# Kernel tuning notes

Hardware: AMD Instinct MI355X
Metric: run time of the kernel (lower is better)

## Reference

```python
import jax, jax.numpy as jnp
import numpy as np

EPS = 1e-5

def conv2d(x, w, stride=1, padding=1, dilation=1):
    # x: [N, C, H, W], w: [O, I, kh, kw]
    return jax.lax.conv_general_dilated(
        x, w, (stride, stride), [(padding, padding), (padding, padding)],
        rhs_dilation=(dilation, dilation),
        dimension_numbers=('NCHW', 'OIHW', 'NCHW'))


def setup_inputs() -> dict:
    key = jax.random.key(0)
    ks = jax.random.split(key, 7)
    T, N, Cin, H, W = 16, 4, 64, 64, 64
    Cout = 64
    x = jax.random.normal(ks[0], (T, N, Cin, H, W), dtype=jnp.float32)
    gamma = jnp.ones((Cin,), jnp.float32)
    beta = jnp.zeros((Cin,), jnp.float32)
    conv1_w = jax.random.normal(ks[1], (3 * Cout, Cin, 3, 3), jnp.float32) * 0.02
    conv1_b = jax.random.normal(ks[2], (3 * Cout,), jnp.float32) * 0.02
    w_h2h = jax.random.normal(ks[3], (3 * Cout, Cout, 3, 3), jnp.float32) * 0.02
    w_c2h = jax.random.normal(ks[4], (3 * Cout, Cout, 3, 3), jnp.float32) * 0.02
    return {"x": x, "gamma": gamma, "beta": beta, "conv1_w": conv1_w,
            "conv1_b": conv1_b, "w_h2h": w_h2h, "w_c2h": w_c2h}


def reference(x, gamma, beta, conv1_w, conv1_b, w_h2h, w_c2h):
    T, N, Cin, H, W = x.shape
    Cout = w_h2h.shape[1]
    # time_to_batch: [T, N, C, H, W] -> [T*N, C, H, W]
    xb = x.reshape(T * N, Cin, H, W)
    # BatchNorm2d (training mode: biased batch stats over N*T, H, W)
    mean = jnp.mean(xb, axis=(0, 2, 3), keepdims=True)
    var = jnp.var(xb, axis=(0, 2, 3), keepdims=True)
    g = gamma.reshape(1, Cin, 1, 1)
    b = beta.reshape(1, Cin, 1, 1)
    bnx = (xb - mean) * jax.lax.rsqrt(var + EPS) * g + b
    # conv1: Cin -> 3*Cout
    y = conv2d(bnx, conv1_w, stride=1, padding=1) + conv1_b.reshape(1, -1, 1, 1)
    # batch_to_time: -> [T, N, 3*Cout, H, W]
    y = y.reshape(T, N, 3 * Cout, H, W)

    # ConvLSTMCell: zero init state is exact (h2h/c2h convs have no bias)
    h0 = jnp.zeros((N, Cout, H, W), y.dtype)
    c0 = jnp.zeros((N, Cout, H, W), y.dtype)

    def step(carry, yt):
        h, c = carry
        tmp = conv2d(c, w_c2h, padding=1) + conv2d(h, w_h2h, padding=1) + yt
        cc_f, cc_o, cc_g = jnp.split(tmp, 3, axis=1)
        f = jax.nn.sigmoid(cc_f)
        o = jax.nn.sigmoid(cc_o)
        gg = jnp.tanh(cc_g)
        c_new = f * c + (1.0 - f) * gg
        h_new = o * jnp.tanh(c_new)
        return (h_new, c_new), h_new

    _, hs = jax.lax.scan(step, (h0, c0), y)
    return hs  # [T, N, Cout, H, W]
```

## Files before the change

kernel.cpp:

```cpp
#include <hip/hip_runtime.h>

typedef unsigned short u16;
typedef unsigned int   u32;
typedef __attribute__((ext_vector_type(8))) short short8;
typedef __attribute__((ext_vector_type(4))) float f32x4;

typedef __attribute__((address_space(1))) const void GASV;
typedef __attribute__((address_space(3))) void LASV;

#define IMG_BYTES  557568
#define WS_SCALE   0
#define WS_SHIFT   256
#define WS_BTAB    512
#define WS_PART2   7424
#define WS_WA      8704
#define WS_BNXP    672256
#define WS_HC      (WS_BNXP + (size_t)64*IMG_BYTES)
#define WS_CSTATE  (WS_HC + (size_t)16*IMG_BYTES)
#define WS_PARTB   (WS_CSTATE + 4194304ULL)

#define SM_RING_OFF 33792
#define SMEM_TOT    (33792 + 6*12288)

__device__ __forceinline__ u16 f2b(float f){
  u32 x = __float_as_uint(f);
  return (u16)((x + 0x7fffu + ((x>>16)&1u)) >> 16);
}
__device__ __forceinline__ float b2f(u16 u){ return __uint_as_float(((u32)u)<<16); }
__device__ __forceinline__ float sigm(float x){ return 1.f/(1.f+__expf(-x)); }
__device__ __forceinline__ float tanh_(float x){
  float e = __expf(2.f*fabsf(x));
  float t = 1.f - 2.f/(e+1.f);
  return copysignf(t, x);
}

__global__ void k_wt(const float* __restrict__ c1, const float* __restrict__ c2h,
                     const float* __restrict__ h2h, const float* __restrict__ scale,
                     u16* __restrict__ wA){
  int idx = blockIdx.x*256 + threadIdx.x;
  int e = idx & 7;
  int lane = (idx >> 3) & 63;
  int v = idx >> 9;
  int f2 = v % 12;  v /= 12;
  int oh = v & 1;
  int stage = v >> 1;
  int cc = f2 / 6, gate = (f2 % 6) >> 1, og2 = f2 & 1;
  int j = stage / 9, tap = stage % 9;
  int och = gate*64 + (oh*2 + og2)*16 + (lane & 15);
  int c = cc*32 + (lane >> 4)*8 + e;
  const float* src = (j==0) ? c1 : ((j==1) ? c2h : h2h);
  float vv = src[(och*64 + c)*9 + tap];
  if (j == 0) vv *= scale[c];
  wA[idx] = f2b(vv);
}

__global__ void k_xt(const float* __restrict__ x, char* __restrict__ xp){
  int img = blockIdx.x / 66, rp = blockIdx.x % 66;
  int tid = threadIdx.x;
  char* dstrow = xp + (size_t)img*IMG_BYTES + (size_t)rp*8448;
  const uint4 z = {0,0,0,0};
  if (rp == 0 || rp == 65){
    for (int i = tid; i < 528; i += 256) ((uint4*)dstrow)[i] = z;
    return;
  }
  if (tid < 16)
    *(uint4*)(dstrow + (tid>>3)*(65*128) + (tid&7)*16) = z;
  int r = rp - 1;
  int col = tid & 63, cq = tid >> 6;
  const float* xb = x + (((size_t)(img*64 + cq*16)) << 12) + (r<<6) + col;
  union { u16 u[16]; uint4 v[2]; } pk;
  #pragma unroll
  for (int i = 0; i < 16; ++i)
    pk.u[i] = f2b(xb[((size_t)i) << 12]);
  char* dst = dstrow + (size_t)(col + 1)*128 + cq*32;
  *(uint4*)dst = pk.v[0];
  *(uint4*)(dst+16) = pk.v[1];
}

__global__ void k_stats(const char* __restrict__ xp, float* __restrict__ part){
  int img = blockIdx.x >> 2, rq = blockIdx.x & 3;
  int tid = threadIdx.x;
  int ch = tid & 7, cell0 = tid >> 3;
  float s[8], q[8];
  #pragma unroll
  for (int i = 0; i < 8; ++i){ s[i] = 0.f; q[i] = 0.f; }
  const char* base = xp + (size_t)img*IMG_BYTES + (size_t)(rq*16+1)*8448 + 128;
  for (int p = 0; p < 32; ++p){
    int cell = p*32 + cell0;
    int rr = cell >> 6, cc = cell & 63;
    uint4 v = *(const uint4*)(base + (size_t)rr*8448 + (size_t)cc*128 + ch*16);
    const u16* u = (const u16*)&v;
    #pragma unroll
    for (int i = 0; i < 8; ++i){
      float f = b2f(u[i]);
      s[i] += f; q[i] += f*f;
    }
  }
  #pragma unroll
  for (int i = 0; i < 8; ++i){
    #pragma unroll
    for (int off = 8; off < 64; off <<= 1){
      s[i] += __shfl_down(s[i], off);
      q[i] += __shfl_down(q[i], off);
    }
  }
  __shared__ float red[4][8][17];
  int w = tid >> 6, lane = tid & 63;
  if (lane < 8){
    #pragma unroll
    for (int i = 0; i < 8; ++i){
      red[w][lane][i]   = s[i];
      red[w][lane][8+i] = q[i];
    }
  }
  __syncthreads();
  if (tid < 128){
    int c = tid & 63, sq = tid >> 6;
    float acc = 0.f;
    #pragma unroll
    for (int wv = 0; wv < 4; ++wv)
      acc += red[wv][c>>3][sq*8 + (c&7)];
    part[(size_t)blockIdx.x*128 + sq*64 + c] = acc;
  }
}

__global__ void k_red(const float* __restrict__ part, float* __restrict__ part2){
  int b = blockIdx.x;
  float s = part[(size_t)threadIdx.x*128 + b];
  #pragma unroll
  for (int off = 32; off; off >>= 1) s += __shfl_down(s, off);
  __shared__ float red[4];
  int w = threadIdx.x >> 6, lane = threadIdx.x & 63;
  if (lane == 0) red[w] = s;
  __syncthreads();
  if (threadIdx.x == 0) part2[b] = red[0]+red[1]+red[2]+red[3];
}

__global__ void k_bnfin(const float* __restrict__ part2, const float* __restrict__ gamma,
                        const float* __restrict__ beta, float* __restrict__ scale,
                        float* __restrict__ shift){
  int c = threadIdx.x;
  const float inv = 1.f/262144.f;
  float mean = part2[c]*inv;
  float var  = part2[64+c]*inv - mean*mean;
  float sc = gamma[c] * rsqrtf(var + 1e-5f);
  scale[c] = sc;
  shift[c] = beta[c] - mean*sc;
}

__global__ void k_bias(const float* __restrict__ c1w, const float* __restrict__ c1b,
                       const float* __restrict__ shift, float* __restrict__ btab){
  int o = blockIdx.x, c = threadIdx.x;
  const float* wp = c1w + (o*64 + c)*9;
  float sh = shift[c];
  float tap[9];
  #pragma unroll
  for (int k = 0; k < 9; ++k) tap[k] = sh*wp[k];
  #pragma unroll
  for (int k = 0; k < 9; ++k){
    #pragma unroll
    for (int off = 32; off; off >>= 1)
      tap[k] += __shfl_down(tap[k], off);
  }
  if (c == 0){
    float b = c1b[o];
    #pragma unroll
    for (int cls = 0; cls < 9; ++cls){
      int rc = cls/3, cl = cls%3;
      int kh0 = (rc==0)?1:0, kh1 = (rc==2)?1:2;
      int kw0 = (cl==0)?1:0, kw1 = (cl==2)?1:2;
      float sm = b;
      for (int kh = kh0; kh <= kh1; ++kh)
        for (int kw = kw0; kw <= kw1; ++kw)
          sm += tap[kh*3+kw];
      btab[cls*192 + o] = sm;
    }
  }
}

#define STAGE_W(v) do {                                                         \
  if ((v) <= 26 && w < 4){                                                      \
    int _vj = jp + (v)/9; if (_vj >= 3) _vj -= 3;                               \
    int _vt = tp + (v)%9; if (_vt >= 9) _vt -= 9;                               \
    const char* _gs = wA + ((size_t)((_vj*9 + _vt)*2 + oh))*12288               \
                        + w*3072 + lane*16;                                     \
    char* _ls = smem + SM_RING_OFF + ((v)%6)*12288 + w*3072;                    \
    __builtin_amdgcn_global_load_lds((GASV*)(_gs),        (LASV*)(_ls),        16, 0, 0); \
    __builtin_amdgcn_global_load_lds((GASV*)(_gs + 1024), (LASV*)(_ls + 1024), 16, 0, 0); \
    __builtin_amdgcn_global_load_lds((GASV*)(_gs + 2048), (LASV*)(_ls + 2048), 16, 0, 0); \
  }                                                                             \
} while(0)

#define WAITN_BAR(N) do {                                                       \
  asm volatile("s_waitcnt vmcnt(" #N ")\n\ts_barrier" ::: "memory");            \
  __builtin_amdgcn_sched_barrier(0);                                            \
} while(0)

#define COMPUTE(u) do {                                                         \
  int tv = tp + (u)%9; if (tv >= 9) tv -= 9;                                    \
  const int kh = tv/3, kw = tv - kh*3;                                          \
  const char* ab0 = smem + SM_RING_OFF + ((u)%6)*12288 + og2*1024 + lane*16;    \
  const int c_ = (ch<<5) + kw + l15;                                            \
  const char* rowb = smem + (wr + kh)*8448 + c_*128;                            \
  _Pragma("unroll")                                                             \
  for (int cc = 0; cc < 2; ++cc){                                               \
    short8 af = *(const short8*)(ab0 + cc*6144);                                \
    short8 ao = *(const short8*)(ab0 + cc*6144 + 2048);                         \
    short8 ag = *(const short8*)(ab0 + cc*6144 + 4096);                         \
    const char* ib0 = rowb + ((((cc<<2)|l4) ^ (c_&7))<<4);                      \
    _Pragma("unroll")                                                           \
    for (int cf = 0; cf < 2; ++cf){                                             \
      short8 bf = *(const short8*)(ib0 + (cf<<11));                             \
      acc[0][cf] = __builtin_amdgcn_mfma_f32_16x16x32_bf16(af, bf, acc[0][cf], 0,0,0); \
      acc[1][cf] = __builtin_amdgcn_mfma_f32_16x16x32_bf16(ao, bf, acc[1][cf], 0,0,0); \
      acc[2][cf] = __builtin_amdgcn_mfma_f32_16x16x32_bf16(ag, bf, acc[2][cf], 0,0,0); \
    }                                                                           \
  }                                                                             \
} while(0)

__global__ __launch_bounds__(512, 1) void k_step(
    const char* __restrict__ bnxp,
    const char* __restrict__ cpad_s, const char* __restrict__ hpad_s,
    char* __restrict__ cpad_d, char* __restrict__ hpad_d,
    const char* __restrict__ wA, const float* __restrict__ btab,
    float* __restrict__ cstate, float* __restrict__ out, int t)
{
  extern __shared__ __align__(16) char smem[];
  const int tid = threadIdx.x;
  const int w = tid >> 6, lane = tid & 63;
  const int l15 = lane & 15, l4 = lane >> 4;
  const int wr = w >> 2, og2 = (w >> 1) & 1, ch = w & 1;
  const int bid = blockIdx.x;
  const int oh = bid & 1, rp = (bid >> 1) & 31, n = bid >> 6;
  const int jp = bid % 3, tp = bid % 9;
  const int r = (rp << 1) + wr;

  const char* gb0 = bnxp   + (size_t)(t*4+n)*IMG_BYTES + rp*16896;
  const char* gb1 = cpad_s + (size_t)n*IMG_BYTES + rp*16896;
  const char* gb2 = hpad_s + (size_t)n*IMG_BYTES + rp*16896;

  float* cslot = cstate + ((size_t)bid*512 + tid)*8;
  float cpv[8];
  if (t == 0){
    #pragma unroll
    for (int i = 0; i < 8; ++i) cpv[i] = 0.f;
  } else {
    f32x4 c0 = *(const f32x4*)cslot;
    f32x4 c1v = *(const f32x4*)(cslot + 4);
    cpv[0]=c0[0]; cpv[1]=c0[1]; cpv[2]=c0[2]; cpv[3]=c0[3];
    cpv[4]=c1v[0]; cpv[5]=c1v[1]; cpv[6]=c1v[2]; cpv[7]=c1v[3];
  }

  const int gc0 = ((oh<<1) + og2)*16 + l4*4;
  const int rc = (r==0) ? 0 : ((r==63) ? 2 : 1);
  const float* btr = btab + rc*576;
  float bv2[2][12];
  #pragma unroll
  for (int cf = 0; cf < 2; ++cf){
    const int col = (ch<<5) + (cf<<4) + l15;
    const int ccl = (col==0) ? 0 : ((col==63) ? 2 : 1);
    const float* bb = btr + ccl*192;
    #pragma unroll
    for (int reg = 0; reg < 4; ++reg){
      bv2[cf][reg]   = bb[gc0+reg];
      bv2[cf][4+reg] = bb[64+gc0+reg];
      bv2[cf][8+reg] = bb[128+gc0+reg];
    }
  }

  f32x4 acc[3][2];
  #pragma unroll
  for (int a = 0; a < 3; ++a)
    #pragma unroll
    for (int b = 0; b < 2; ++b)
      acc[a][b] = (f32x4){0.f,0.f,0.f,0.f};

  STAGE_W(0); STAGE_W(1); STAGE_W(2); STAGE_W(3);

  #pragma unroll
  for (int jj = 0; jj < 3; ++jj){
    int jv = jp + jj; if (jv >= 3) jv -= 3;
    const char* gbj = (jv==0) ? gb0 : ((jv==1) ? gb1 : gb2);
    for (int i = tid; i < 2112; i += 512){
      int rr = i / 528;
      int iw = i - rr*528;
      int c = iw >> 3, k = iw & 7;
      *(uint4*)(smem + rr*8448 + c*128 + ((k ^ (c&7))<<4)) =
          *(const uint4*)(gbj + rr*8448 + iw*16);
    }
    __syncthreads();

    #pragma unroll
    for (int pp = 0; pp < 4; ++pp){
      const int u = jj*9 + 2*pp;
      STAGE_W(u+4); STAGE_W(u+5);
      __builtin_amdgcn_s_setprio(1);
      COMPUTE(u);
      COMPUTE(u+1);
      __builtin_amdgcn_s_setprio(0);
      if (u == 22)      WAITN_BAR(3);
      else if (u == 24) WAITN_BAR(0);
      else              WAITN_BAR(6);
    }
    {
      const int u = jj*9 + 8;
      STAGE_W(u+4);
      __builtin_amdgcn_s_setprio(1);
      COMPUTE(u);
      __builtin_amdgcn_s_setprio(0);
    }
  }

  const size_t ob = ((size_t)((t*4+n)*64)) << 12;
  char* hrow = hpad_d + (size_t)n*IMG_BYTES + (size_t)(r+1)*8448;
  char* crow = cpad_d + (size_t)n*IMG_BYTES + (size_t)(r+1)*8448;

  float cnew[8];
  #pragma unroll
  for (int cf = 0; cf < 2; ++cf){
    const int col = (ch<<5) + (cf<<4) + l15;
    const int p = (r<<6) + col;
    union { u16 u[4]; uint2 v; } hp, cp2;
    #pragma unroll
    for (int reg = 0; reg < 4; ++reg){
      const int gc = gc0 + reg;
      float f  = sigm(acc[0][cf][reg] + bv2[cf][reg]);
      float og_ = sigm(acc[1][cf][reg] + bv2[cf][4+reg]);
      float g  = tanh_(acc[2][cf][reg] + bv2[cf][8+reg]);
      float cn = f*cpv[cf*4+reg] + (1.f-f)*g;
      float hn = og_ * tanh_(cn);
      cnew[cf*4+reg] = cn;
      out[ob + (((size_t)gc)<<12) + p] = hn;
      hp.u[reg]  = f2b(hn);
      cp2.u[reg] = f2b(cn);
    }
    *(uint2*)(hrow + (size_t)(col+1)*128 + gc0*2) = hp.v;
    *(uint2*)(crow + (size_t)(col+1)*128 + gc0*2) = cp2.v;
  }
  *(f32x4*)cslot       = (f32x4){cnew[0],cnew[1],cnew[2],cnew[3]};
  *(f32x4*)(cslot + 4) = (f32x4){cnew[4],cnew[5],cnew[6],cnew[7]};
}

extern "C" void kernel_launch(void* const* d_in, const int* in_sizes, int n_in,
                              void* d_out, int out_size, void* d_ws, size_t ws_size,
                              hipStream_t stream)
{
  (void)in_sizes; (void)n_in; (void)out_size; (void)ws_size;
  const float* x     = (const float*)d_in[0];
  const float* gamma = (const float*)d_in[1];
  const float* beta  = (const float*)d_in[2];
  const float* c1w   = (const float*)d_in[3];
  const float* c1b   = (const float*)d_in[4];
  const float* wh2h  = (const float*)d_in[5];
  const float* wc2h  = (const float*)d_in[6];
  char* ws  = (char*)d_ws;
  float* out = (float*)d_out;

  hipFuncSetAttribute(reinterpret_cast<const void*>(k_step),
                      hipFuncAttributeMaxDynamicSharedMemorySize, SMEM_TOT);

  char* hpad0 = ws + WS_HC;
  char* cpad0 = ws + WS_HC + (size_t)4*IMG_BYTES;
  char* hpad1 = ws + WS_HC + (size_t)8*IMG_BYTES;
  char* cpad1 = ws + WS_HC + (size_t)12*IMG_BYTES;

  hipMemsetAsync(ws + WS_HC, 0, (size_t)16*IMG_BYTES, stream);

  k_xt<<<4224, 256, 0, stream>>>(x, ws + WS_BNXP);
  k_stats<<<256, 256, 0, stream>>>(ws + WS_BNXP, (float*)(ws + WS_PARTB));
  k_red<<<128, 256, 0, stream>>>((const float*)(ws + WS_PARTB),
                                 (float*)(ws + WS_PART2));
  k_bnfin<<<1, 64, 0, stream>>>((const float*)(ws + WS_PART2), gamma, beta,
                                (float*)(ws + WS_SCALE), (float*)(ws + WS_SHIFT));
  k_wt<<<1296, 256, 0, stream>>>(c1w, wc2h, wh2h,
                                 (const float*)(ws + WS_SCALE), (u16*)(ws + WS_WA));
  k_bias<<<192, 64, 0, stream>>>(c1w, c1b, (const float*)(ws + WS_SHIFT),
                                 (float*)(ws + WS_BTAB));

  for (int t = 0; t < 16; ++t){
    const char* cs = (t & 1) ? cpad1 : cpad0;
    const char* hs = (t & 1) ? hpad1 : hpad0;
    char* cd = (t & 1) ? cpad0 : cpad1;
    char* hd = (t & 1) ? hpad0 : hpad1;
    k_step<<<256, 512, SMEM_TOT, stream>>>(ws + WS_BNXP, cs, hs, cd, hd,
                                           ws + WS_WA,
                                           (const float*)(ws + WS_BTAB),
                                           (float*)(ws + WS_CSTATE), out, t);
  }
}
```

Before: 356.2 us.

## Drop LDS staging in step kernel; load weights and inputs straight from global

Removes the shared-memory ring that staged weights and the swizzled shared-memory copy of the input rows. Each wave now loads its A fragments (weights) into registers with double buffering and reads B fragments directly from global memory, with no barriers. This removes the LDS copy traffic and synchronisation cost. The trade-off is that every wave issues redundant global and L2 reads of the same weights and overlapping input rows, and exposes global load latency in front of the MFMAs.

```diff
diff --git a/kernel.cpp b/kernel.cpp
--- a/kernel.cpp
+++ b/kernel.cpp
@@ -4,9 +4,6 @@
 typedef unsigned int   u32;
 typedef __attribute__((ext_vector_type(8))) short short8;
 typedef __attribute__((ext_vector_type(4))) float f32x4;
-
-typedef __attribute__((address_space(1))) const void GASV;
-typedef __attribute__((address_space(3))) void LASV;
 
 #define IMG_BYTES  557568
 #define WS_SCALE   0
@@ -18,9 +15,6 @@
 #define WS_HC      (WS_BNXP + (size_t)64*IMG_BYTES)
 #define WS_CSTATE  (WS_HC + (size_t)16*IMG_BYTES)
 #define WS_PARTB   (WS_CSTATE + 4194304ULL)
-
-#define SM_RING_OFF 33792
-#define SMEM_TOT    (33792 + 6*12288)
 
 __device__ __forceinline__ u16 f2b(float f){
   u32 x = __float_as_uint(f);
@@ -178,42 +172,33 @@
   }
 }
 
-#define STAGE_W(v) do {                                                         \
-  if ((v) <= 26 && w < 4){                                                      \
-    int _vj = jp + (v)/9; if (_vj >= 3) _vj -= 3;                               \
-    int _vt = tp + (v)%9; if (_vt >= 9) _vt -= 9;                               \
-    const char* _gs = wA + ((size_t)((_vj*9 + _vt)*2 + oh))*12288               \
-                        + w*3072 + lane*16;                                     \
-    char* _ls = smem + SM_RING_OFF + ((v)%6)*12288 + w*3072;                    \
-    __builtin_amdgcn_global_load_lds((GASV*)(_gs),        (LASV*)(_ls),        16, 0, 0); \
-    __builtin_amdgcn_global_load_lds((GASV*)(_gs + 1024), (LASV*)(_ls + 1024), 16, 0, 0); \
-    __builtin_amdgcn_global_load_lds((GASV*)(_gs + 2048), (LASV*)(_ls + 2048), 16, 0, 0); \
-  }                                                                             \
+#define LOADA(BUF, v) do {                                                      \
+  int vj_ = jp + (v)/9; if (vj_ >= 3) vj_ -= 3;                                 \
+  int vt_ = tp + (v)%9; if (vt_ >= 9) vt_ -= 9;                                 \
+  const char* ap_ = wA + ((size_t)((vj_*9 + vt_)*2 + oh))*12288                 \
+                       + (og2<<10) + (lane<<4);                                 \
+  BUF[0] = *(const short8*)(ap_);                                               \
+  BUF[1] = *(const short8*)(ap_ + 2048);                                        \
+  BUF[2] = *(const short8*)(ap_ + 4096);                                        \
+  BUF[3] = *(const short8*)(ap_ + 6144);                                        \
+  BUF[4] = *(const short8*)(ap_ + 8192);                                        \
+  BUF[5] = *(const short8*)(ap_ + 10240);                                       \
 } while(0)
 
-#define WAITN_BAR(N) do {                                                       \
-  asm volatile("s_waitcnt vmcnt(" #N ")\n\ts_barrier" ::: "memory");            \
-  __builtin_amdgcn_sched_barrier(0);                                            \
-} while(0)
-
-#define COMPUTE(u) do {                                                         \
-  int tv = tp + (u)%9; if (tv >= 9) tv -= 9;                                    \
-  const int kh = tv/3, kw = tv - kh*3;                                          \
-  const char* ab0 = smem + SM_RING_OFF + ((u)%6)*12288 + og2*1024 + lane*16;    \
-  const int c_ = (ch<<5) + kw + l15;                                            \
-  const char* rowb = smem + (wr + kh)*8448 + c_*128;                            \
+#define COMPUTEG(BUF, v) do {                                                   \
+  int vj_ = jp + (v)/9; if (vj_ >= 3) vj_ -= 3;                                 \
+  int vt_ = tp + (v)%9; if (vt_ >= 9) vt_ -= 9;                                 \
+  const int kh_ = vt_/3, kw_ = vt_ - kh_*3;                                     \
+  const char* gbj_ = (vj_==0) ? gb0 : ((vj_==1) ? gb1 : gb2);                   \
+  const char* bb_ = gbj_ + kh_*8448 + kw_*128 + broff;                          \
   _Pragma("unroll")                                                             \
   for (int cc = 0; cc < 2; ++cc){                                               \
-    short8 af = *(const short8*)(ab0 + cc*6144);                                \
-    short8 ao = *(const short8*)(ab0 + cc*6144 + 2048);                         \
-    short8 ag = *(const short8*)(ab0 + cc*6144 + 4096);                         \
-    const char* ib0 = rowb + ((((cc<<2)|l4) ^ (c_&7))<<4);                      \
     _Pragma("unroll")                                                           \
     for (int cf = 0; cf < 2; ++cf){                                             \
-      short8 bf = *(const short8*)(ib0 + (cf<<11));                             \
-      acc[0][cf] = __builtin_amdgcn_mfma_f32_16x16x32_bf16(af, bf, acc[0][cf], 0,0,0); \
-      acc[1][cf] = __builtin_amdgcn_mfma_f32_16x16x32_bf16(ao, bf, acc[1][cf], 0,0,0); \
-      acc[2][cf] = __builtin_amdgcn_mfma_f32_16x16x32_bf16(ag, bf, acc[2][cf], 0,0,0); \
+      short8 bf = *(const short8*)(bb_ + (cc<<6) + (cf<<11));                   \
+      acc[0][cf] = __builtin_amdgcn_mfma_f32_16x16x32_bf16(BUF[cc*3+0], bf, acc[0][cf], 0,0,0); \
+      acc[1][cf] = __builtin_amdgcn_mfma_f32_16x16x32_bf16(BUF[cc*3+1], bf, acc[1][cf], 0,0,0); \
+      acc[2][cf] = __builtin_amdgcn_mfma_f32_16x16x32_bf16(BUF[cc*3+2], bf, acc[2][cf], 0,0,0); \
     }                                                                           \
   }                                                                             \
 } while(0)
@@ -225,7 +210,6 @@
     const char* __restrict__ wA, const float* __restrict__ btab,
     float* __restrict__ cstate, float* __restrict__ out, int t)
 {
-  extern __shared__ __align__(16) char smem[];
   const int tid = threadIdx.x;
   const int w = tid >> 6, lane = tid & 63;
   const int l15 = lane & 15, l4 = lane >> 4;
@@ -235,9 +219,28 @@
   const int jp = bid % 3, tp = bid % 9;
   const int r = (rp << 1) + wr;
 
-  const char* gb0 = bnxp   + (size_t)(t*4+n)*IMG_BYTES + rp*16896;
-  const char* gb1 = cpad_s + (size_t)n*IMG_BYTES + rp*16896;
-  const char* gb2 = hpad_s + (size_t)n*IMG_BYTES + rp*16896;
+  const char* gb0 = bnxp   + (size_t)(t*4+n)*IMG_BYTES + rp*16896 + wr*8448;
+  const char* gb1 = cpad_s + (size_t)n*IMG_BYTES + rp*16896 + wr*8448;
+  const char* gb2 = hpad_s + (size_t)n*IMG_BYTES + rp*16896 + wr*8448;
+  const int broff = ((ch<<5) + l15)*128 + (l4<<4);
+
+  f32x4 acc[3][2];
+  #pragma unroll
+  for (int a = 0; a < 3; ++a)
+    #pragma unroll
+    for (int b = 0; b < 2; ++b)
+      acc[a][b] = (f32x4){0.f,0.f,0.f,0.f};
+
+  short8 a0[6], a1[6];
+  LOADA(a0, 0);
+  #pragma unroll
+  for (int s = 0; s < 13; ++s){
+    LOADA(a1, 2*s+1);
+    COMPUTEG(a0, 2*s);
+    LOADA(a0, 2*s+2);
+    COMPUTEG(a1, 2*s+1);
+  }
+  COMPUTEG(a0, 26);
 
   float* cslot = cstate + ((size_t)bid*512 + tid)*8;
   float cpv[8];
@@ -250,66 +253,9 @@
     cpv[0]=c0[0]; cpv[1]=c0[1]; cpv[2]=c0[2]; cpv[3]=c0[3];
     cpv[4]=c1v[0]; cpv[5]=c1v[1]; cpv[6]=c1v[2]; cpv[7]=c1v[3];
   }
-
   const int gc0 = ((oh<<1) + og2)*16 + l4*4;
   const int rc = (r==0) ? 0 : ((r==63) ? 2 : 1);
   const float* btr = btab + rc*576;
-  float bv2[2][12];
-  #pragma unroll
-  for (int cf = 0; cf < 2; ++cf){
-    const int col = (ch<<5) + (cf<<4) + l15;
-    const int ccl = (col==0) ? 0 : ((col==63) ? 2 : 1);
-    const float* bb = btr + ccl*192;
-    #pragma unroll
-    for (int reg = 0; reg < 4; ++reg){
-      bv2[cf][reg]   = bb[gc0+reg];
-      bv2[cf][4+reg] = bb[64+gc0+reg];
-      bv2[cf][8+reg] = bb[128+gc0+reg];
-    }
-  }
-
-  f32x4 acc[3][2];
-  #pragma unroll
-  for (int a = 0; a < 3; ++a)
-    #pragma unroll
-    for (int b = 0; b < 2; ++b)
-      acc[a][b] = (f32x4){0.f,0.f,0.f,0.f};
-
-  STAGE_W(0); STAGE_W(1); STAGE_W(2); STAGE_W(3);
-
-  #pragma unroll
-  for (int jj = 0; jj < 3; ++jj){
-    int jv = jp + jj; if (jv >= 3) jv -= 3;
-    const char* gbj = (jv==0) ? gb0 : ((jv==1) ? gb1 : gb2);
-    for (int i = tid; i < 2112; i += 512){
-      int rr = i / 528;
-      int iw = i - rr*528;
-      int c = iw >> 3, k = iw & 7;
-      *(uint4*)(smem + rr*8448 + c*128 + ((k ^ (c&7))<<4)) =
-          *(const uint4*)(gbj + rr*8448 + iw*16);
-    }
-    __syncthreads();
-
-    #pragma unroll
-    for (int pp = 0; pp < 4; ++pp){
-      const int u = jj*9 + 2*pp;
-      STAGE_W(u+4); STAGE_W(u+5);
-      __builtin_amdgcn_s_setprio(1);
-      COMPUTE(u);
-      COMPUTE(u+1);
-      __builtin_amdgcn_s_setprio(0);
-      if (u == 22)      WAITN_BAR(3);
-      else if (u == 24) WAITN_BAR(0);
-      else              WAITN_BAR(6);
-    }
-    {
-      const int u = jj*9 + 8;
-      STAGE_W(u+4);
-      __builtin_amdgcn_s_setprio(1);
-      COMPUTE(u);
-      __builtin_amdgcn_s_setprio(0);
-    }
-  }
 
   const size_t ob = ((size_t)((t*4+n)*64)) << 12;
   char* hrow = hpad_d + (size_t)n*IMG_BYTES + (size_t)(r+1)*8448;
@@ -320,13 +266,15 @@
   for (int cf = 0; cf < 2; ++cf){
     const int col = (ch<<5) + (cf<<4) + l15;
     const int p = (r<<6) + col;
+    const int ccl = (col==0) ? 0 : ((col==63) ? 2 : 1);
+    const float* bb = btr + ccl*192;
     union { u16 u[4]; uint2 v; } hp, cp2;
     #pragma unroll
     for (int reg = 0; reg < 4; ++reg){
       const int gc = gc0 + reg;
-      float f  = sigm(acc[0][cf][reg] + bv2[cf][reg]);
-      float og_ = sigm(acc[1][cf][reg] + bv2[cf][4+reg]);
-      float g  = tanh_(acc[2][cf][reg] + bv2[cf][8+reg]);
+      float f  = sigm(acc[0][cf][reg] + bb[gc]);
+      float og_ = sigm(acc[1][cf][reg] + bb[64+gc]);
+      float g  = tanh_(acc[2][cf][reg] + bb[128+gc]);
       float cn = f*cpv[cf*4+reg] + (1.f-f)*g;
       float hn = og_ * tanh_(cn);
       cnew[cf*4+reg] = cn;
@@ -356,9 +304,6 @@
   char* ws  = (char*)d_ws;
   float* out = (float*)d_out;
 
-  hipFuncSetAttribute(reinterpret_cast<const void*>(k_step),
-                      hipFuncAttributeMaxDynamicSharedMemorySize, SMEM_TOT);
-
   char* hpad0 = ws + WS_HC;
   char* cpad0 = ws + WS_HC + (size_t)4*IMG_BYTES;
   char* hpad1 = ws + WS_HC + (size_t)8*IMG_BYTES;
@@ -382,9 +327,9 @@
     const char* hs = (t & 1) ? hpad1 : hpad0;
     char* cd = (t & 1) ? cpad0 : cpad1;
     char* hd = (t & 1) ? hpad0 : hpad1;
-    k_step<<<256, 512, SMEM_TOT, stream>>>(ws + WS_BNXP, cs, hs, cd, hd,
-                                           ws + WS_WA,
-                                           (const float*)(ws + WS_BTAB),
-                                           (float*)(ws + WS_CSTATE), out, t);
-  }
-}
+    k_step<<<256, 512, 0, stream>>>(ws + WS_BNXP, cs, hs, cd, hd,
+                                    ws + WS_WA,
+                                    (const float*)(ws + WS_BTAB),
+                                    (float*)(ws + WS_CSTATE), out, t);
+  }
+}
```

Result: slower. 675.9 us (+89.7%).
